# Optimization experiments

Measured on AMD Instinct MI355X. Metric: run time of the kernel, lower is better.

The kernel has to match this reference:

```python
import jax, jax.numpy as jnp
import numpy as np

A = 2
IMG_C = 3
IMG_H = 64
IMG_W = 96
N_OBJ = 5   # OBJS + STACKS with REMOVE_BG
B = 64
P = 4       # number of predicate nets
CONV_OUT = 32


def setup_inputs() -> dict:
    key = jax.random.key(0)
    k0, k1, k2, k3 = jax.random.split(key, 4)
    state = jax.random.normal(k0, (B, N_OBJ, IMG_C, IMG_H, IMG_W), jnp.float32)
    state_next = jax.random.normal(k1, (B, N_OBJ, IMG_C, IMG_H, IMG_W), jnp.float32)
    # uniform object count (structural max N=5) so tuple count is static
    n_obj = jnp.full((B,), N_OBJ, dtype=jnp.int32)
    temp = jnp.float32(0.5)
    # stacked params for the P predicate nets (conv + linear head)
    conv_w = jax.random.normal(k2, (P * CONV_OUT, A * IMG_C, 3, 3), jnp.float32) * 0.05
    conv_b = jnp.zeros((P * CONV_OUT,), jnp.float32)
    w2 = jax.random.normal(k3, (P, CONV_OUT), jnp.float32) * 0.1
    b2 = jnp.zeros((P,), jnp.float32)
    return {"state": state, "state_next": state_next, "conv_w": conv_w,
            "conv_b": conv_b, "w2": w2, "b2": b2, "n_obj": n_obj, "temp": temp}


def _build_tuples(s, n):
    # cartesian_prod(arange(n), arange(n)) -> ordered pairs (i, j)
    ii = jnp.repeat(jnp.arange(n), n)   # [n*n]
    jj = jnp.tile(jnp.arange(n), n)     # [n*n]
    a = s[:, ii]                        # [B, n*n, C, H, W]
    b = s[:, jj]
    t = jnp.concatenate([a, b], axis=2)             # [B, n*n, A*C, H, W]
    return t.reshape(-1, A * IMG_C, IMG_H, IMG_W)   # [B*n*n, 6, H, W]


def _predicates(t, conv_w, conv_b, w2, b2, temp):
    # fused conv over all P nets (stacked output channels)
    y = jax.lax.conv_general_dilated(
        t, conv_w, window_strides=(2, 2), padding='SAME',
        dimension_numbers=('NCHW', 'OIHW', 'NCHW'))
    y = jax.nn.relu(y + conv_b[None, :, None, None])
    y = y.mean(axis=(2, 3)).reshape(-1, P, CONV_OUT)   # [T, P, 32]
    logits = jnp.einsum('tpc,pc->tp', y, w2) + b2      # [T, P]
    return jax.nn.sigmoid(logits / temp)


def reference(state, state_next, conv_w, conv_b, w2, b2, n_obj, temp):
    n = N_OBJ  # uniform ragged case: all n_obj entries equal the max
    tuples = _build_tuples(state, n)
    tuples_next = _build_tuples(state_next, n)
    preds = _predicates(tuples, conv_w, conv_b, w2, b2, temp)
    preds_next = _predicates(tuples_next, conv_w, conv_b, w2, b2, temp)
    # adjacency: column per tuple, one-hot in the owning sample's row
    T = B * n * n
    adj = (jnp.arange(T)[None, :] // (n * n) == jnp.arange(B)[:, None]).astype(jnp.float32)
    return preds, preds_next, adj
```

## Files before the change

kernel.cpp:

```cpp
#include <hip/hip_runtime.h>
#include <math.h>

#define BQ 64
#define NOBJ 5
#define CIN 3
#define IMG_H 64
#define IMG_W 96
#define OH 32
#define OW 48
#define NPAIR 25
#define PP 4
#define CONV_OUT 32

#define NRG 16
#define NPOS 96
#define XK 32
#define X_U32 (NOBJ * NPOS * XK / 2)
#define X_UNITS (NOBJ * NPOS * 4)

#define NPRED (2 * 1600 * PP)
#define ADJ_N (BQ * 1600)

typedef __fp16   h2 __attribute__((ext_vector_type(2)));
typedef _Float16 half8 __attribute__((ext_vector_type(8)));
typedef float    float4_ __attribute__((ext_vector_type(4)));
typedef unsigned int uint4_ __attribute__((ext_vector_type(4)));

__global__ __launch_bounds__(512) void conv_pair_mfma(
    const float* __restrict__ state,
    const float* __restrict__ state_next,
    const float* __restrict__ conv_w,
    const float* __restrict__ conv_b,
    const float* __restrict__ w2,
    float* __restrict__ T,
    float* __restrict__ out)
{
    __shared__ __align__(16) unsigned int sX32[X_U32];

    const int tid = threadIdx.x;
    const int rg  = blockIdx.x;
    const int b   = blockIdx.y;
    const int src = blockIdx.z;

    const float* g = (src == 0 ? state : state_next)
                   + (size_t)b * NOBJ * CIN * IMG_H * IMG_W;
    const int R0 = rg * 4;

    if (src == 1 && tid < 100) {
        int a  = (rg + NRG * b) * 100 + tid;
        int bb = a / 1600;
        int t  = a - bb * 1600;
        out[NPRED + a] = (t / NPAIR == bb) ? 1.0f : 0.0f;
    }

    const int wave = tid >> 6;
    const int lane = tid & 63;
    const int quad = lane >> 4;
    const int ocl  = lane & 15;

    const int mt  = wave;
    const int p   = mt >> 1;
    const int row = mt * 16 + ocl;

    half8 wa, wb;
    #pragma unroll
    for (int j = 0; j < 8; ++j) {
        int k = quad * 8 + j;
        float va = 0.f, vb = 0.f;
        if (k < 27) {
            va = conv_w[row * 54 + k];
            vb = conv_w[row * 54 + 27 + k];
        } else if (k == 27) {
            va = conv_b[row];
        }
        wa[j] = (_Float16)va;
        wb[j] = (_Float16)vb;
    }
    h2 w2h01, w2h23;
    {
        const float* wp = w2 + p * CONV_OUT + (mt & 1) * 16 + quad * 4;
        w2h01 = __builtin_amdgcn_cvt_pkrtz(wp[0], wp[1]);
        w2h23 = __builtin_amdgcn_cvt_pkrtz(wp[2], wp[3]);
    }

    {
        const int subk = tid & 3;
        int koff[8], khv[8], kwv[8];
        float padf[8];
        bool kval[8];
        #pragma unroll
        for (int j = 0; j < 8; ++j) {
            int k = subk * 8 + j;
            if (k < 27) {
                int ci = k / 9;
                int r9 = k - ci * 9;
                int kh = r9 / 3;
                int kw = r9 - kh * 3;
                koff[j] = ci * (IMG_H * IMG_W) + kh * IMG_W + kw;
                khv[j] = kh; kwv[j] = kw; kval[j] = true; padf[j] = 0.f;
            } else {
                koff[j] = 0; khv[j] = 0; kwv[j] = 0; kval[j] = false;
                padf[j] = (k == 27) ? 1.0f : 0.f;
            }
        }
        for (int u = tid; u < X_UNITS; u += 512) {
            int pl  = (u >> 2) % NPOS;
            int obj = u / (NPOS * 4);
            int rl  = (pl >= 48) ? 1 : 0;
            int pc  = pl - rl * 48;
            int gr0 = R0 + 2 * rl;
            int gc0 = 2 * pc;
            const float* gp = g + obj * (CIN * IMG_H * IMG_W) + gr0 * IMG_W + gc0;
            float fv[8];
            #pragma unroll
            for (int j = 0; j < 8; ++j) {
                float v = padf[j];
                if (kval[j] && (gr0 + khv[j] < IMG_H) && (gc0 + kwv[j] < IMG_W))
                    v = gp[koff[j]];
                fv[j] = v;
            }
            uint4_ w4;
            w4.x = __builtin_bit_cast(unsigned int, __builtin_amdgcn_cvt_pkrtz(fv[0], fv[1]));
            w4.y = __builtin_bit_cast(unsigned int, __builtin_amdgcn_cvt_pkrtz(fv[2], fv[3]));
            w4.z = __builtin_bit_cast(unsigned int, __builtin_amdgcn_cvt_pkrtz(fv[4], fv[5]));
            w4.w = __builtin_bit_cast(unsigned int, __builtin_amdgcn_cvt_pkrtz(fv[6], fv[7]));
            *(uint4_*)&sX32[(size_t)u * 4] = w4;
        }
    }

    __syncthreads();

    const float4_ zero4 = {0.f, 0.f, 0.f, 0.f};
    const h2 hz = {(__fp16)0.f, (__fp16)0.f};

    float acc[NPAIR];
    #pragma unroll
    for (int q = 0; q < NPAIR; ++q) acc[q] = 0.f;

    #pragma unroll
    for (int nt = 0; nt < 6; ++nt) {
        const int rl  = nt / 3;
        const int c0  = (nt - rl * 3) * 16;
        const int pos = rl * 48 + c0 + ocl;

        half8 xf[NOBJ];
        h2 ah01[NOBJ], ah23[NOBJ];
        #pragma unroll
        for (int obj = 0; obj < NOBJ; ++obj) {
            xf[obj] = *(const half8*)&sX32[((size_t)(obj * NPOS + pos)) * 16 + quad * 4];
            float4_ a = __builtin_amdgcn_mfma_f32_16x16x32_f16(wa, xf[obj], zero4, 0, 0, 0);
            ah01[obj] = __builtin_amdgcn_cvt_pkrtz(a[0], a[1]);
            ah23[obj] = __builtin_amdgcn_cvt_pkrtz(a[2], a[3]);
        }

        #pragma unroll
        for (int jo = 0; jo < NOBJ; ++jo) {
            float4_ bq = __builtin_amdgcn_mfma_f32_16x16x32_f16(wb, xf[jo], zero4, 0, 0, 0);
            h2 bh01 = __builtin_amdgcn_cvt_pkrtz(bq[0], bq[1]);
            h2 bh23 = __builtin_amdgcn_cvt_pkrtz(bq[2], bq[3]);
            #pragma unroll
            for (int i = 0; i < NOBJ; ++i) {
                h2 s0 = ah01[i] + bh01;
                h2 s1 = ah23[i] + bh23;
                s0 = __builtin_elementwise_max(s0, hz);
                s1 = __builtin_elementwise_max(s1, hz);
                float t0 = __builtin_amdgcn_fdot2(s0, w2h01, acc[i * NOBJ + jo], false);
                acc[i * NOBJ + jo] = __builtin_amdgcn_fdot2(s1, w2h23, t0, false);
            }
        }
    }

    float myv = 0.f;
    #pragma unroll
    for (int q = 0; q < NPAIR; ++q) {
        float rr = acc[q];
        #pragma unroll
        for (int off = 32; off > 0; off >>= 1)
            rr += __shfl_xor(rr, off, 64);
        if (lane == q) myv = rr;
    }
    if (lane < NPAIR)
        T[((((size_t)src * BQ + b) * NRG + rg) * NPAIR + lane) * 8 + mt] = myv;
}

__global__ __launch_bounds__(256) void pred_kernel(
    const float* __restrict__ T,
    const float* __restrict__ b2,
    const float* __restrict__ temp,
    float* __restrict__ out)
{
    int idx = blockIdx.x * blockDim.x + threadIdx.x;
    if (idx >= NPRED) return;
    int p   = idx & 3;
    int t   = (idx >> 2) % 1600;
    int src = idx / 6400;
    int bb  = t / NPAIR;
    int pr  = t - bb * NPAIR;
    const float* base = T + ((((size_t)src * BQ + bb) * NRG) * NPAIR + pr) * 8 + 2 * p;
    float sum = 0.f;
    #pragma unroll
    for (int rgi = 0; rgi < NRG; ++rgi) {
        sum += base[(size_t)rgi * NPAIR * 8];
        sum += base[(size_t)rgi * NPAIR * 8 + 1];
    }
    float logit = sum * (1.0f / (OH * OW)) + b2[p];
    float x = logit / temp[0];
    out[idx] = 1.0f / (1.0f + expf(-x));
}

extern "C" void kernel_launch(void* const* d_in, const int* in_sizes, int n_in,
                              void* d_out, int out_size, void* d_ws, size_t ws_size,
                              hipStream_t stream)
{
    const float* state      = (const float*)d_in[0];
    const float* state_next = (const float*)d_in[1];
    const float* conv_w     = (const float*)d_in[2];
    const float* conv_b     = (const float*)d_in[3];
    const float* w2         = (const float*)d_in[4];
    const float* b2         = (const float*)d_in[5];
    const float* temp       = (const float*)d_in[7];

    float* out = (float*)d_out;
    float* T   = (float*)d_ws;

    dim3 grid1(NRG, BQ, 2);
    conv_pair_mfma<<<grid1, 512, 0, stream>>>(state, state_next, conv_w, conv_b,
                                              w2, T, out);

    pred_kernel<<<(NPRED + 255) / 256, 256, 0, stream>>>(T, b2, temp, out);
}
```

Baseline: 152.5 us.

## Fuse prediction epilogue into conv kernel via atomics and last-block reduction

Drops the separate pred_kernel. Each block now atomically adds its per-pair partial sums into a small workspace, and the last of the 16 row-group blocks per sample (found with an atomic counter) applies bias, temperature and sigmoid. The LDS layout of the im2col tile is also XOR-swizzled to reduce bank conflicts on the half8 reads. In exchange it adds a memset launch, atomic traffic, threadfences, and float-atomic summation order that is not deterministic.

After: 460.6 us. +202.0%, slower.

```diff
diff --git a/kernel.cpp b/kernel.cpp
--- a/kernel.cpp
+++ b/kernel.cpp
@@ -20,22 +20,27 @@
 
 #define NPRED (2 * 1600 * PP)
 #define ADJ_N (BQ * 1600)
+#define S_FLOATS (2 * BQ * NPAIR * PP)
 
 typedef __fp16   h2 __attribute__((ext_vector_type(2)));
 typedef _Float16 half8 __attribute__((ext_vector_type(8)));
 typedef float    float4_ __attribute__((ext_vector_type(4)));
 typedef unsigned int uint4_ __attribute__((ext_vector_type(4)));
 
-__global__ __launch_bounds__(512) void conv_pair_mfma(
+__global__ __launch_bounds__(512) void conv_pair_fused(
     const float* __restrict__ state,
     const float* __restrict__ state_next,
     const float* __restrict__ conv_w,
     const float* __restrict__ conv_b,
     const float* __restrict__ w2,
-    float* __restrict__ T,
+    const float* __restrict__ b2,
+    const float* __restrict__ temp,
+    float* __restrict__ S,
+    unsigned int* __restrict__ cnt,
     float* __restrict__ out)
 {
     __shared__ __align__(16) unsigned int sX32[X_U32];
+    __shared__ int islast;
 
     const int tid = threadIdx.x;
     const int rg  = blockIdx.x;
@@ -124,7 +129,8 @@
             w4.y = __builtin_bit_cast(unsigned int, __builtin_amdgcn_cvt_pkrtz(fv[2], fv[3]));
             w4.z = __builtin_bit_cast(unsigned int, __builtin_amdgcn_cvt_pkrtz(fv[4], fv[5]));
             w4.w = __builtin_bit_cast(unsigned int, __builtin_amdgcn_cvt_pkrtz(fv[6], fv[7]));
-            *(uint4_*)&sX32[(size_t)u * 4] = w4;
+            int swk = subk ^ ((pl >> 1) & 3);
+            *(uint4_*)&sX32[(size_t)(obj * (NPOS * 16) + pl * 16 + swk * 4)] = w4;
         }
     }
 
@@ -142,12 +148,14 @@
         const int rl  = nt / 3;
         const int c0  = (nt - rl * 3) * 16;
         const int pos = rl * 48 + c0 + ocl;
+        const int sw  = (pos >> 1) & 3;
+        const int sbase = pos * 16 + ((quad ^ sw) << 2);
 
         half8 xf[NOBJ];
         h2 ah01[NOBJ], ah23[NOBJ];
         #pragma unroll
         for (int obj = 0; obj < NOBJ; ++obj) {
-            xf[obj] = *(const half8*)&sX32[((size_t)(obj * NPOS + pos)) * 16 + quad * 4];
+            xf[obj] = *(const half8*)&sX32[sbase + obj * (NPOS * 16)];
             float4_ a = __builtin_amdgcn_mfma_f32_16x16x32_f16(wa, xf[obj], zero4, 0, 0, 0);
             ah01[obj] = __builtin_amdgcn_cvt_pkrtz(a[0], a[1]);
             ah23[obj] = __builtin_amdgcn_cvt_pkrtz(a[2], a[3]);
@@ -179,33 +187,30 @@
             rr += __shfl_xor(rr, off, 64);
         if (lane == q) myv = rr;
     }
+
+    const size_t sbidx = ((size_t)src * BQ + b);
     if (lane < NPAIR)
-        T[((((size_t)src * BQ + b) * NRG + rg) * NPAIR + lane) * 8 + mt] = myv;
-}
-
-__global__ __launch_bounds__(256) void pred_kernel(
-    const float* __restrict__ T,
-    const float* __restrict__ b2,
-    const float* __restrict__ temp,
-    float* __restrict__ out)
-{
-    int idx = blockIdx.x * blockDim.x + threadIdx.x;
-    if (idx >= NPRED) return;
-    int p   = idx & 3;
-    int t   = (idx >> 2) % 1600;
-    int src = idx / 6400;
-    int bb  = t / NPAIR;
-    int pr  = t - bb * NPAIR;
-    const float* base = T + ((((size_t)src * BQ + bb) * NRG) * NPAIR + pr) * 8 + 2 * p;
-    float sum = 0.f;
-    #pragma unroll
-    for (int rgi = 0; rgi < NRG; ++rgi) {
-        sum += base[(size_t)rgi * NPAIR * 8];
-        sum += base[(size_t)rgi * NPAIR * 8 + 1];
-    }
-    float logit = sum * (1.0f / (OH * OW)) + b2[p];
-    float x = logit / temp[0];
-    out[idx] = 1.0f / (1.0f + expf(-x));
+        atomicAdd(&S[(sbidx * NPAIR + lane) * PP + p], myv);
+
+    __threadfence();
+    __syncthreads();
+    if (tid == 0) {
+        unsigned int old = atomicAdd(&cnt[sbidx], 1u);
+        islast = (old == NRG - 1);
+    }
+    __syncthreads();
+
+    if (islast && tid < NPAIR * PP) {
+        __threadfence();
+        int pair = tid >> 2;
+        int pp   = tid & 3;
+        float s = __hip_atomic_load(&S[(sbidx * NPAIR + pair) * PP + pp],
+                                    __ATOMIC_RELAXED, __HIP_MEMORY_SCOPE_AGENT);
+        float logit = s * (1.0f / (OH * OW)) + b2[pp];
+        float x = logit / temp[0];
+        out[(size_t)src * 6400 + ((size_t)b * NPAIR + pair) * PP + pp] =
+            1.0f / (1.0f + expf(-x));
+    }
 }
 
 extern "C" void kernel_launch(void* const* d_in, const int* in_sizes, int n_in,
@@ -221,11 +226,12 @@
     const float* temp       = (const float*)d_in[7];
 
     float* out = (float*)d_out;
-    float* T   = (float*)d_ws;
+    float* S   = (float*)d_ws;
+    unsigned int* cnt = (unsigned int*)(S + S_FLOATS);
+
+    hipMemsetAsync(d_ws, 0, (S_FLOATS + 2 * BQ) * sizeof(float), stream);
 
     dim3 grid1(NRG, BQ, 2);
-    conv_pair_mfma<<<grid1, 512, 0, stream>>>(state, state_next, conv_w, conv_b,
-                                              w2, T, out);
-
-    pred_kernel<<<(NPRED + 255) / 256, 256, 0, stream>>>(T, b2, temp, out);
+    conv_pair_fused<<<grid1, 512, 0, stream>>>(state, state_next, conv_w, conv_b,
+                                               w2, b2, temp, S, cnt, out);
 }
```
